# Optimization experiments

Hardware: AMD Instinct MI355X
Metric: run time of the kernel (lower is better)

The kernel has to match this reference:

```python
import jax, jax.numpy as jnp
import numpy as np

L, D_IN, D_HID, D_OUT, N = 8, 256, 1024, 256, 32768


def setup_inputs() -> dict:
    key = jax.random.key(0)
    kx, kp, kw1, kw2 = jax.random.split(key, 4)
    x = jax.random.normal(kx, (N, D_IN), dtype=jnp.float32)
    plane_idx = jax.random.randint(kp, (N,), 0, L, dtype=jnp.int32)
    W1 = jax.random.normal(kw1, (L, D_HID, D_IN), dtype=jnp.float32) * 0.014
    b1 = jnp.zeros((L, D_HID), dtype=jnp.float32)
    W2 = jax.random.normal(kw2, (L, D_OUT, D_HID), dtype=jnp.float32) * np.float32((2.0 / D_HID) ** 0.5)
    b2 = jnp.zeros((L, D_OUT), dtype=jnp.float32)
    return {"x": x, "W1": W1, "b1": b1, "W2": W2, "b2": b2, "plane_idx": plane_idx}


def reference(x, W1, b1, W2, b2, plane_idx):
    # Dense-dispatch MoE reference: scan over the L planes, run the full
    # 2-layer MLP for each plane's weights, and select per-walker rows via
    # the plane mask (equivalent math to gather -> MLP -> scatter).
    n_planes = W1.shape[0]
    out0 = jnp.zeros((x.shape[0], W2.shape[1]), dtype=x.dtype)

    def plane_step(out, p):
        h = jax.nn.gelu(x @ W1[p].T + b1[p], approximate=False)  # [N, D_hid]
        o = h @ W2[p].T + b2[p]                                  # [N, D_out]
        out = jnp.where((plane_idx == p)[:, None], o, out)
        return out, None

    out, _ = jax.lax.scan(plane_step, out0, jnp.arange(n_planes))
    return out
```

## Files before the change

### kernel.cpp

```cpp
#include <hip/hip_runtime.h>
#include <hip/hip_fp16.h>
#include <cstdint>

#define NT      32768
#define DIN     256
#define DHID    1024
#define DOUT    256
#define NPLANES 8
#define NBLK    (NT / 256)

typedef unsigned short u16;
typedef __attribute__((ext_vector_type(8))) _Float16 f16x8;
typedef __attribute__((ext_vector_type(4))) float    f32x4;

#define WS_OFFSETS 0
#define WS_META    64
#define WS_TP      1024
#define WS_TM      (WS_TP + 544*4)
#define WS_BLKHIST (WS_TM + 544*4)
#define WS_PERM    (WS_BLKHIST + NBLK*8*4)
#define WS_XB      (WS_PERM + NT*4)
#define WS_W1B     (WS_XB + NT*DIN*2)
#define WS_W2B     (WS_W1B + NPLANES*DHID*DIN*2)
#define WS_HB      (WS_W2B + NPLANES*DOUT*DHID*2)

__device__ __forceinline__ u16 f2h_bits(float f) {
    __half h = __float2half(f);
    return *reinterpret_cast<u16*>(&h);
}

__device__ __forceinline__ void gl_lds16(const void* g, void* l) {
    __builtin_amdgcn_global_load_lds(
        (const __attribute__((address_space(1))) void*)g,
        (__attribute__((address_space(3))) void*)l,
        16, 0, 0);
}

__device__ __forceinline__ float gelu_fast(float x) {
    const float u = x * (1.5957691216f + 0.07135481283f * x * x);
    const float e = __expf(-u);
    return x * __builtin_amdgcn_rcpf(1.0f + e);
}

__global__ void prep_k(const int* __restrict__ pidx, const float* __restrict__ x,
                       const float* __restrict__ W1, const float* __restrict__ W2,
                       int* __restrict__ blkhist, u16* __restrict__ xb,
                       u16* __restrict__ w1b, u16* __restrict__ w2b) {
    __shared__ int cnt[NPLANES];
    const int t = threadIdx.x, lane = t & 63;
    if ((int)blockIdx.x < NBLK) {
        if (t < NPLANES) cnt[t] = 0;
        __syncthreads();
        const int p = pidx[blockIdx.x * 256 + t];
#pragma unroll
        for (int q = 0; q < NPLANES; ++q) {
            unsigned long long m = __ballot(p == q);
            if (p == q && __popcll(m & ((1ULL << lane) - 1)) == 0)
                atomicAdd(&cnt[q], __popcll(m));
        }
        __syncthreads();
        if (t < NPLANES) blkhist[blockIdx.x * NPLANES + t] = cnt[t];
    }
    const int n0 = NT * DIN / 4, n1 = NPLANES * DHID * DIN / 4, n2 = NPLANES * DOUT * DHID / 4;
    const int stride = gridDim.x * blockDim.x;
    for (int i = blockIdx.x * blockDim.x + t; i < n0 + n1 + n2; i += stride) {
        const float4* s; ushort4* d; int j;
        if (i < n0)           { s = (const float4*)x;  d = (ushort4*)xb;  j = i; }
        else if (i < n0 + n1) { s = (const float4*)W1; d = (ushort4*)w1b; j = i - n0; }
        else                  { s = (const float4*)W2; d = (ushort4*)w2b; j = i - n0 - n1; }
        float4 v = s[j];
        ushort4 o;
        o.x = f2h_bits(v.x); o.y = f2h_bits(v.y);
        o.z = f2h_bits(v.z); o.w = f2h_bits(v.w);
        d[j] = o;
    }
}

__global__ void scatter_k(const int* __restrict__ pidx, const int* __restrict__ blkhist,
                          int* __restrict__ offsets, int* __restrict__ meta,
                          int* __restrict__ tp, int* __restrict__ tm,
                          int* __restrict__ perm) {
    __shared__ int stot[NPLANES], spre[NPLANES], sbase[NPLANES];
    __shared__ int wcnt[4][NPLANES], wbase[4][NPLANES];
    const int t = threadIdx.x, lane = t & 63, wave = t >> 6;
    if (t < NPLANES) {
        int tot = 0, pre = 0;
        for (int b = 0; b < NBLK; ++b) {
            const int v = blkhist[b * NPLANES + t];
            tot += v;
            if (b < (int)blockIdx.x) pre += v;
        }
        stot[t] = tot; spre[t] = pre;
    }
    __syncthreads();
    if (t == 0) {
        int run = 0;
        for (int q = 0; q < NPLANES; ++q) {
            sbase[q] = run + spre[q];
            if (blockIdx.x == 0) offsets[q] = run;
            run += stot[q];
        }
        if (blockIdx.x == 0) offsets[NPLANES] = run;
    }
    __syncthreads();
    if (blockIdx.x == 0 && t < NPLANES) {
        int pre = 0, ntiles = 0;
#pragma unroll
        for (int q = 0; q < NPLANES; ++q) {
            const int ntq = (stot[q] + 63) >> 6;
            if (q < t) pre += ntq;
            ntiles += ntq;
        }
        for (int m = 0, i = pre; m < stot[t]; m += 64, ++i) { tp[i] = t; tm[i] = m; }
        if (t == 0) meta[0] = ntiles;
    }
    const int i = blockIdx.x * 256 + t;
    const int p = pidx[i];
    int rank = 0;
#pragma unroll
    for (int q = 0; q < NPLANES; ++q) {
        unsigned long long m = __ballot(p == q);
        if (lane == 0) wcnt[wave][q] = __popcll(m);
        if (p == q) rank = __popcll(m & ((1ULL << lane) - 1));
    }
    __syncthreads();
    if (t < NPLANES) {
        int run = sbase[t];
#pragma unroll
        for (int w = 0; w < 4; ++w) { wbase[w][t] = run; run += wcnt[w][t]; }
    }
    __syncthreads();
    perm[wbase[wave][p] + rank] = i;
}

#define XCD_MAP(NSPLIT)                                                        \
    const int ntiles = meta[0];                                                \
    const int xcd = blockIdx.x & 7, idx = blockIdx.x >> 3;                     \
    const int q8 = ntiles >> 3, r8 = ntiles & 7;                               \
    const int tn = q8 + (xcd < r8 ? 1 : 0);                                    \
    if (idx >= tn * (NSPLIT)) return;                                          \
    const int tile = (xcd < r8 ? xcd * (q8 + 1)                                \
                               : r8 * (q8 + 1) + (xcd - r8) * q8)              \
                     + idx / (NSPLIT);                                         \
    const int sub = idx % (NSPLIT);                                            \
    const int p   = tp[tile];                                                  \
    const int m0  = tm[tile];                                                  \
    const int off = offsets[p];                                                \
    const int cnt = offsets[p + 1] - off;

__global__ __launch_bounds__(256, 6) void gemm1_k(
    const u16* __restrict__ xb, const u16* __restrict__ w1b,
    const float* __restrict__ b1, const int* __restrict__ perm,
    const int* __restrict__ offsets, const int* __restrict__ meta,
    const int* __restrict__ tp, const int* __restrict__ tm,
    u16* __restrict__ hb)
{
    __shared__ __align__(16) u16 smem[12288];
    XCD_MAP(8)
    const int n0v = sub * 128;

    u16* const sA = smem;
    u16* const sB = smem + 4096;

    const int tid = threadIdx.x;
    const u16* aptr[2];
    const u16* bptr[4];
#pragma unroll
    for (int c = 0; c < 2; ++c) {
        const int slot = c * 256 + tid, row = slot >> 3, ch = slot & 7;
        const int gr = min(m0 + row, cnt - 1);
        aptr[c] = xb + (size_t)perm[off + gr] * DIN + ((ch ^ (row & 7)) * 8);
    }
#pragma unroll
    for (int c = 0; c < 4; ++c) {
        const int slot = c * 256 + tid, row = slot >> 3, ch = slot & 7;
        bptr[c] = w1b + ((size_t)p * DHID + n0v + row) * DIN + ((ch ^ (row & 7)) * 8);
    }
    const int wave = tid >> 6, lane = tid & 63;
    const int wr = wave >> 1, wc = wave & 1;
    const int lm = lane & 15, lk = lane >> 4;

    f32x4 acc[2][4];
#pragma unroll
    for (int a = 0; a < 2; ++a)
#pragma unroll
        for (int b = 0; b < 4; ++b) acc[a][b] = (f32x4){0.f, 0.f, 0.f, 0.f};

    for (int kt = 0; kt < DIN / 64; ++kt) {
        const int k0 = kt * 64;
#pragma unroll
        for (int c = 0; c < 2; ++c) gl_lds16(aptr[c] + k0, sA + c * 2048 + tid * 8);
#pragma unroll
        for (int c = 0; c < 4; ++c) gl_lds16(bptr[c] + k0, sB + c * 2048 + tid * 8);
        __syncthreads();
#pragma unroll
        for (int kk = 0; kk < 2; ++kk) {
            f16x8 af[2], bf[4];
#pragma unroll
            for (int mf = 0; mf < 2; ++mf) {
                const int row = wr * 32 + mf * 16 + lm;
                const int g   = kk * 4 + lk;
                af[mf] = *(const f16x8*)(sA + row * 64 + ((g ^ (row & 7)) * 8));
            }
#pragma unroll
            for (int nf = 0; nf < 4; ++nf) {
                const int row = wc * 64 + nf * 16 + lm;
                const int g   = kk * 4 + lk;
                bf[nf] = *(const f16x8*)(sB + row * 64 + ((g ^ (row & 7)) * 8));
            }
#pragma unroll
            for (int mf = 0; mf < 2; ++mf)
#pragma unroll
                for (int nf = 0; nf < 4; ++nf)
                    acc[mf][nf] = __builtin_amdgcn_mfma_f32_16x16x32_f16(
                        af[mf], bf[nf], acc[mf][nf], 0, 0, 0);
        }
        __syncthreads();
    }

    u16* const sOut = smem;
#pragma unroll
    for (int nf = 0; nf < 4; ++nf) {
        const int col = wc * 64 + nf * 16 + lm;
        const float bb = b1[p * DHID + n0v + col];
        const int cc = col >> 3, c7 = col & 7;
#pragma unroll
        for (int mf = 0; mf < 2; ++mf) {
#pragma unroll
            for (int j = 0; j < 4; ++j) {
                const int tok = wr * 32 + mf * 16 + lk * 4 + j;
                sOut[tok * 128 + ((cc ^ (tok & 15)) * 8) + c7] =
                    f2h_bits(gelu_fast(acc[mf][nf][j] + bb));
            }
        }
    }
    __syncthreads();
    const int r = tid >> 2, qq = tid & 3;
    if (m0 + r < cnt) {
        u16* dst = hb + (size_t)(off + m0 + r) * DHID + n0v;
#pragma unroll
        for (int c = 0; c < 4; ++c) {
            const int l = qq * 4 + c;
            *(int4*)(dst + l * 8) = *(const int4*)(sOut + r * 128 + ((l ^ (r & 15)) * 8));
        }
    }
}

__global__ __launch_bounds__(256, 6) void gemm2_k(
    const u16* __restrict__ hb, const u16* __restrict__ w2b,
    const float* __restrict__ b2, const int* __restrict__ perm,
    const int* __restrict__ offsets, const int* __restrict__ meta,
    const int* __restrict__ tp, const int* __restrict__ tm,
    float* __restrict__ out)
{
    __shared__ __align__(16) u16 smem[12288];
    XCD_MAP(2)
    const int n0v = sub * 128;

    u16* const sA = smem;
    u16* const sB = smem + 4096;

    const int tid = threadIdx.x;
    const u16* aptr[2];
    const u16* bptr[4];
#pragma unroll
    for (int c = 0; c < 2; ++c) {
        const int slot = c * 256 + tid, row = slot >> 3, ch = slot & 7;
        aptr[c] = hb + (size_t)(off + min(m0 + row, cnt - 1)) * DHID + ((ch ^ (row & 7)) * 8);
    }
#pragma unroll
    for (int c = 0; c < 4; ++c) {
        const int slot = c * 256 + tid, row = slot >> 3, ch = slot & 7;
        bptr[c] = w2b + ((size_t)p * DOUT + n0v + row) * DHID + ((ch ^ (row & 7)) * 8);
    }
    const int wave = tid >> 6, lane = tid & 63;
    const int wr = wave >> 1, wc = wave & 1;
    const int lm = lane & 15, lk = lane >> 4;

    f32x4 acc[2][4];
#pragma unroll
    for (int a = 0; a < 2; ++a)
#pragma unroll
        for (int b = 0; b < 4; ++b) acc[a][b] = (f32x4){0.f, 0.f, 0.f, 0.f};

    for (int kt = 0; kt < DHID / 64; ++kt) {
        const int k0 = kt * 64;
#pragma unroll
        for (int c = 0; c < 2; ++c) gl_lds16(aptr[c] + k0, sA + c * 2048 + tid * 8);
#pragma unroll
        for (int c = 0; c < 4; ++c) gl_lds16(bptr[c] + k0, sB + c * 2048 + tid * 8);
        __syncthreads();
#pragma unroll
        for (int kk = 0; kk < 2; ++kk) {
            f16x8 af[2], bf[4];
#pragma unroll
            for (int mf = 0; mf < 2; ++mf) {
                const int row = wr * 32 + mf * 16 + lm;
                const int g   = kk * 4 + lk;
                af[mf] = *(const f16x8*)(sA + row * 64 + ((g ^ (row & 7)) * 8));
            }
#pragma unroll
            for (int nf = 0; nf < 4; ++nf) {
                const int row = wc * 64 + nf * 16 + lm;
                const int g   = kk * 4 + lk;
                bf[nf] = *(const f16x8*)(sB + row * 64 + ((g ^ (row & 7)) * 8));
            }
#pragma unroll
            for (int mf = 0; mf < 2; ++mf)
#pragma unroll
                for (int nf = 0; nf < 4; ++nf)
                    acc[mf][nf] = __builtin_amdgcn_mfma_f32_16x16x32_f16(
                        af[mf], bf[nf], acc[mf][nf], 0, 0, 0);
        }
        __syncthreads();
    }

#pragma unroll
    for (int nf = 0; nf < 4; ++nf) {
        const int col = n0v + wc * 64 + nf * 16 + lm;
        const float bb = b2[p * DOUT + col];
#pragma unroll
        for (int mf = 0; mf < 2; ++mf) {
#pragma unroll
            for (int j = 0; j < 4; ++j) {
                const int tok = wr * 32 + mf * 16 + lk * 4 + j;
                if (m0 + tok < cnt)
                    out[(size_t)perm[off + m0 + tok] * DOUT + col] = acc[mf][nf][j] + bb;
            }
        }
    }
}

extern "C" void kernel_launch(void* const* d_in, const int* in_sizes, int n_in,
                              void* d_out, int out_size, void* d_ws, size_t ws_size,
                              hipStream_t stream) {
    const float* x    = (const float*)d_in[0];
    const float* W1   = (const float*)d_in[1];
    const float* b1   = (const float*)d_in[2];
    const float* W2   = (const float*)d_in[3];
    const float* b2   = (const float*)d_in[4];
    const int*   pidx = (const int*)d_in[5];
    float*       out  = (float*)d_out;

    char* ws      = (char*)d_ws;
    int* offsets  = (int*)(ws + WS_OFFSETS);
    int* meta     = (int*)(ws + WS_META);
    int* tp       = (int*)(ws + WS_TP);
    int* tm       = (int*)(ws + WS_TM);
    int* blkhist  = (int*)(ws + WS_BLKHIST);
    int* perm     = (int*)(ws + WS_PERM);
    u16* xb       = (u16*)(ws + WS_XB);
    u16* w1b      = (u16*)(ws + WS_W1B);
    u16* w2b      = (u16*)(ws + WS_W2B);
    u16* hb       = (u16*)(ws + WS_HB);

    prep_k<<<2048, 256, 0, stream>>>(pidx, x, W1, W2, blkhist, xb, w1b, w2b);
    scatter_k<<<NBLK, 256, 0, stream>>>(pidx, blkhist, offsets, meta, tp, tm, perm);

    gemm1_k<<<4224, 256, 0, stream>>>(xb, w1b, b1, perm, offsets, meta, tp, tm, hb);
    gemm2_k<<<1056, 256, 0, stream>>>(hb, w2b, b2, perm, offsets, meta, tp, tm, out);
}
```

Before: 102.1 us.

## Double-buffer gemm1 LDS tiles with K=32 prefetch and fenced barriers

Restructures the first GEMM's K loop from single-buffered 64-wide tiles into two ping-pong 32-wide LDS buffers. The next tile's global-to-LDS loads are issued before computing on the current one, and partial vmcnt waits keep them in flight. The aim is to hide global load latency behind MFMA work. In exchange the loop runs twice as many iterations and barriers, and the smaller K tile needs a new 4-chunk swizzle.

```diff
diff --git a/kernel.cpp b/kernel.cpp
--- a/kernel.cpp
+++ b/kernel.cpp
@@ -159,22 +159,16 @@
     XCD_MAP(8)
     const int n0v = sub * 128;
 
-    u16* const sA = smem;
-    u16* const sB = smem + 4096;
-
     const int tid = threadIdx.x;
-    const u16* aptr[2];
-    const u16* bptr[4];
+    const int arow = tid >> 2, ach = tid & 3;
+    const u16* aptr = xb + (size_t)perm[off + min(m0 + arow, cnt - 1)] * DIN
+                         + ((ach ^ ((arow >> 1) & 3)) * 8);
+    const u16* bptr[2];
 #pragma unroll
     for (int c = 0; c < 2; ++c) {
-        const int slot = c * 256 + tid, row = slot >> 3, ch = slot & 7;
-        const int gr = min(m0 + row, cnt - 1);
-        aptr[c] = xb + (size_t)perm[off + gr] * DIN + ((ch ^ (row & 7)) * 8);
-    }
-#pragma unroll
-    for (int c = 0; c < 4; ++c) {
-        const int slot = c * 256 + tid, row = slot >> 3, ch = slot & 7;
-        bptr[c] = w1b + ((size_t)p * DHID + n0v + row) * DIN + ((ch ^ (row & 7)) * 8);
+        const int slot = c * 256 + tid, row = slot >> 2, ch = slot & 3;
+        bptr[c] = w1b + ((size_t)p * DHID + n0v + row) * DIN
+                      + ((ch ^ ((row >> 1) & 3)) * 8);
     }
     const int wave = tid >> 6, lane = tid & 63;
     const int wr = wave >> 1, wc = wave & 1;
@@ -186,37 +180,58 @@
 #pragma unroll
         for (int b = 0; b < 4; ++b) acc[a][b] = (f32x4){0.f, 0.f, 0.f, 0.f};
 
-    for (int kt = 0; kt < DIN / 64; ++kt) {
-        const int k0 = kt * 64;
-#pragma unroll
-        for (int c = 0; c < 2; ++c) gl_lds16(aptr[c] + k0, sA + c * 2048 + tid * 8);
-#pragma unroll
-        for (int c = 0; c < 4; ++c) gl_lds16(bptr[c] + k0, sB + c * 2048 + tid * 8);
-        __syncthreads();
-#pragma unroll
-        for (int kk = 0; kk < 2; ++kk) {
-            f16x8 af[2], bf[4];
-#pragma unroll
-            for (int mf = 0; mf < 2; ++mf) {
-                const int row = wr * 32 + mf * 16 + lm;
-                const int g   = kk * 4 + lk;
-                af[mf] = *(const f16x8*)(sA + row * 64 + ((g ^ (row & 7)) * 8));
-            }
-#pragma unroll
-            for (int nf = 0; nf < 4; ++nf) {
-                const int row = wc * 64 + nf * 16 + lm;
-                const int g   = kk * 4 + lk;
-                bf[nf] = *(const f16x8*)(sB + row * 64 + ((g ^ (row & 7)) * 8));
-            }
-#pragma unroll
-            for (int mf = 0; mf < 2; ++mf)
-#pragma unroll
-                for (int nf = 0; nf < 4; ++nf)
-                    acc[mf][nf] = __builtin_amdgcn_mfma_f32_16x16x32_f16(
-                        af[mf], bf[nf], acc[mf][nf], 0, 0, 0);
-        }
-        __syncthreads();
-    }
+#define STAGE1(buf, kt) do {                                                   \
+        gl_lds16(aptr + (kt) * 32, (buf) + tid * 8);                           \
+        gl_lds16(bptr[0] + (kt) * 32, (buf) + 2048 + tid * 8);                 \
+        gl_lds16(bptr[1] + (kt) * 32, (buf) + 4096 + tid * 8); } while (0)
+
+#define COMPUTE1(buf) do {                                                     \
+        f16x8 af[2], bf[4];                                                    \
+        _Pragma("unroll") for (int mf = 0; mf < 2; ++mf) {                     \
+            const int row = wr * 32 + mf * 16 + lm;                            \
+            af[mf] = *(const f16x8*)((buf) + row * 32 +                        \
+                                     ((lk ^ ((row >> 1) & 3)) * 8));           \
+        }                                                                      \
+        _Pragma("unroll") for (int nf = 0; nf < 4; ++nf) {                     \
+            const int row = wc * 64 + nf * 16 + lm;                            \
+            bf[nf] = *(const f16x8*)((buf) + 2048 + row * 32 +                 \
+                                     ((lk ^ ((row >> 1) & 3)) * 8));           \
+        }                                                                      \
+        _Pragma("unroll") for (int mf = 0; mf < 2; ++mf)                       \
+            _Pragma("unroll") for (int nf = 0; nf < 4; ++nf)                   \
+                acc[mf][nf] = __builtin_amdgcn_mfma_f32_16x16x32_f16(          \
+                    af[mf], bf[nf], acc[mf][nf], 0, 0, 0); } while (0)
+
+#define FENCED_BARRIER() do {                                                  \
+        __builtin_amdgcn_sched_barrier(0);                                     \
+        __builtin_amdgcn_s_barrier();                                          \
+        __builtin_amdgcn_sched_barrier(0); } while (0)
+
+    u16* const buf0 = smem;
+    u16* const buf1 = smem + 6144;
+
+    STAGE1(buf0, 0);
+    asm volatile("s_waitcnt vmcnt(0)" ::: "memory");
+    FENCED_BARRIER();
+
+    constexpr int KT = DIN / 32;
+#pragma unroll
+    for (int kt = 0; kt < KT; ++kt) {
+        u16* const cur = (kt & 1) ? buf1 : buf0;
+        u16* const nxt = (kt & 1) ? buf0 : buf1;
+        if (kt + 1 < KT) {
+            STAGE1(nxt, kt + 1);
+            asm volatile("s_waitcnt vmcnt(3)" ::: "memory");
+        } else {
+            asm volatile("s_waitcnt vmcnt(0)" ::: "memory");
+        }
+        FENCED_BARRIER();
+        COMPUTE1(cur);
+        FENCED_BARRIER();
+    }
+#undef STAGE1
+#undef COMPUTE1
+#undef FENCED_BARRIER
 
     u16* const sOut = smem;
 #pragma unroll
```

Result: slower. 104.7 us (+2.6%).
